# Kernel tuning notes

Measured on AMD Instinct MI355X. Metric: run time of the kernel, lower is better.

## Reference

```python
import jax, jax.numpy as jnp
import numpy as np

B, S, H, E = 4, 4096, 4096, 64
EPS = 1e-6


def setup_inputs() -> dict:
    key = jax.random.key(0)
    k1, k2 = jax.random.split(key)
    hidden_states = jax.random.normal(k1, (B, S, H), dtype=jnp.float32)
    gate_w = jax.random.normal(k2, (E, H), dtype=jnp.float32) * 0.02
    return {"hidden_states": hidden_states, "gate_w": gate_w, "C": 512}


def reference(hidden_states, gate_w, C):
    b, s, h = hidden_states.shape
    e = gate_w.shape[0]
    flat = hidden_states.reshape(-1, h)                    # [BS, H]
    logits = jnp.einsum('th,eh->te', flat, gate_w)          # [BS, E]
    # deterministic=True -> no noise added
    probs = jax.nn.softmax(logits, axis=-1)                 # [BS, E]
    # expert-choice: each expert picks top-C tokens
    _, topC_idx = jax.lax.top_k(logits.T, C)                # [E, C] token indices
    routing_map = jnp.zeros_like(logits).at[
        topC_idx, jnp.arange(e)[:, None]].set(1.0)          # [BS, E]
    # normalize_weights=True
    probs = probs * routing_map
    probs = probs / (probs.sum(axis=-1, keepdims=True) + EPS)
    # aux losses (torch .std() is unbiased -> ddof=1)
    importance = probs.sum(axis=0)                          # [E]
    imp_loss = (jnp.std(importance, ddof=1) / (importance.mean() + EPS)) ** 2
    load = routing_map.sum(axis=0)                          # [E]
    load_loss = (jnp.std(load, ddof=1) / (load.mean() + EPS)) ** 2
    aux_loss = imp_loss + load_loss
    return (probs.reshape(b, s, e), routing_map.reshape(b, s, e), aux_loss)
```

## Files before the change

kernel.cpp:

```cpp
#include <hip/hip_runtime.h>
#include <hip/hip_bf16.h>

#define BS 16384
#define HDIM 4096
#define NE 64
#define KC 64
#define TT 32
#define CAP 512
#define DELTA 2e-3f

typedef __bf16 bf16x8 __attribute__((ext_vector_type(8)));
typedef float f32x4 __attribute__((ext_vector_type(4)));
union Frag { uint4 q; bf16x8 v; };

__device__ inline unsigned f2key(float f) {
    unsigned u = __float_as_uint(f);
    return (u & 0x80000000u) ? ~u : (u | 0x80000000u);
}
__device__ inline float key2f(unsigned k) {
    unsigned u = (k & 0x80000000u) ? (k ^ 0x80000000u) : ~k;
    return __uint_as_float(u);
}
__device__ inline unsigned pack_hi(float a, float b) {
    return (__float_as_uint(a) >> 16) | (__float_as_uint(b) & 0xFFFF0000u);
}
__device__ inline float bf16_resid(float a) {
    return a - __uint_as_float(__float_as_uint(a) & 0xFFFF0000u);
}

__global__ __launch_bounds__(256) void k0_init(const float* __restrict__ W,
                                               unsigned short* __restrict__ Wh,
                                               unsigned short* __restrict__ Wl,
                                               unsigned long long* __restrict__ win_t) {
    const int gtid = blockIdx.x * 256 + threadIdx.x;
    const size_t f = (size_t)gtid * 4;
    float4 w = *(const float4*)(W + f);
    uint2 hh, ll;
    hh.x = pack_hi(w.x, w.y); hh.y = pack_hi(w.z, w.w);
    ll.x = pack_hi(bf16_resid(w.x), bf16_resid(w.y));
    ll.y = pack_hi(bf16_resid(w.z), bf16_resid(w.w));
    *(uint2*)(Wh + f) = hh;
    *(uint2*)(Wl + f) = ll;
    if (gtid < BS) win_t[gtid] = 0ull;
}

__global__ __launch_bounds__(256, 2) void k1_gemm(const float* __restrict__ A,
                                                  const unsigned short* __restrict__ Wh,
                                                  const unsigned short* __restrict__ Wl,
                                                  float* __restrict__ Lg,
                                                  unsigned* __restrict__ KeyT) {
    __shared__ __align__(16) unsigned short sbuf[2 * 13824];

    const int tid = threadIdx.x;
    const int T0 = blockIdx.x * TT;

    const int arow = tid >> 3, aseg = tid & 7;

    const int lane = tid & 63, w = tid >> 6;
    const int m = lane & 15, q = lane >> 4;
    const int wm = w & 1;
    const int wn = w >> 1;

    const float* Aprow = A + (size_t)(T0 + arow) * HDIM + aseg * 8;

    f32x4 acc[2] = {{0.f, 0.f, 0.f, 0.f}, {0.f, 0.f, 0.f, 0.f}};

    float4 pa0 = *(const float4*)(Aprow);
    float4 pa1 = *(const float4*)(Aprow + 4);
    uint4 pwh[2], pwl[2];
#pragma unroll
    for (int i = 0; i < 2; ++i) {
        const int u = i * 256 + tid;
        const int r = u >> 3, blk = u & 7;
        pwh[i] = *(const uint4*)(Wh + (size_t)r * HDIM + blk * 8);
        pwl[i] = *(const uint4*)(Wl + (size_t)r * HDIM + blk * 8);
    }

    {
        unsigned short* B = sbuf;
        uint4 H, L;
        H.x = pack_hi(pa0.x, pa0.y); H.y = pack_hi(pa0.z, pa0.w);
        H.z = pack_hi(pa1.x, pa1.y); H.w = pack_hi(pa1.z, pa1.w);
        L.x = pack_hi(bf16_resid(pa0.x), bf16_resid(pa0.y));
        L.y = pack_hi(bf16_resid(pa0.z), bf16_resid(pa0.w));
        L.z = pack_hi(bf16_resid(pa1.x), bf16_resid(pa1.y));
        L.w = pack_hi(bf16_resid(pa1.z), bf16_resid(pa1.w));
        *(uint4*)(B + arow * 72 + aseg * 8) = H;
        *(uint4*)(B + 2304 + arow * 72 + aseg * 8) = L;
#pragma unroll
        for (int i = 0; i < 2; ++i) {
            const int u = i * 256 + tid;
            const int r = u >> 3, blk = u & 7;
            *(uint4*)(B + 4608 + r * 72 + blk * 8) = pwh[i];
            *(uint4*)(B + 9216 + r * 72 + blk * 8) = pwl[i];
        }
    }

    for (int c = 0; c < HDIM / KC; ++c) {
        if (c + 1 < HDIM / KC) {
            const int c0 = (c + 1) * KC;
            pa0 = *(const float4*)(Aprow + c0);
            pa1 = *(const float4*)(Aprow + c0 + 4);
#pragma unroll
            for (int i = 0; i < 2; ++i) {
                const int u = i * 256 + tid;
                const int r = u >> 3, blk = u & 7;
                pwh[i] = *(const uint4*)(Wh + (size_t)r * HDIM + c0 + blk * 8);
                pwl[i] = *(const uint4*)(Wl + (size_t)r * HDIM + c0 + blk * 8);
            }
        }
        __syncthreads();
        {
            const unsigned short* B = sbuf + (c & 1) * 13824;
            const unsigned short* Ash = B + (wm * 16 + m) * 72;
            const unsigned short* Asl = Ash + 2304;
#pragma unroll
            for (int kh = 0; kh < 2; ++kh) {
                const int ko = kh * 32 + q * 8;
                Frag ah, al;
                ah.q = *(const uint4*)(Ash + ko);
                al.q = *(const uint4*)(Asl + ko);
#pragma unroll
                for (int nt = 0; nt < 2; ++nt) {
                    const int er = wn * 32 + nt * 16 + m;
                    Frag bh, bl;
                    bh.q = *(const uint4*)(B + 4608 + er * 72 + ko);
                    bl.q = *(const uint4*)(B + 9216 + er * 72 + ko);
                    acc[nt] = __builtin_amdgcn_mfma_f32_16x16x32_bf16(ah.v, bh.v, acc[nt], 0, 0, 0);
                    acc[nt] = __builtin_amdgcn_mfma_f32_16x16x32_bf16(al.v, bh.v, acc[nt], 0, 0, 0);
                    acc[nt] = __builtin_amdgcn_mfma_f32_16x16x32_bf16(ah.v, bl.v, acc[nt], 0, 0, 0);
                }
            }
        }
        if (c + 1 < HDIM / KC) {
            unsigned short* B = sbuf + ((c + 1) & 1) * 13824;
            uint4 H, L;
            H.x = pack_hi(pa0.x, pa0.y); H.y = pack_hi(pa0.z, pa0.w);
            H.z = pack_hi(pa1.x, pa1.y); H.w = pack_hi(pa1.z, pa1.w);
            L.x = pack_hi(bf16_resid(pa0.x), bf16_resid(pa0.y));
            L.y = pack_hi(bf16_resid(pa0.z), bf16_resid(pa0.w));
            L.z = pack_hi(bf16_resid(pa1.x), bf16_resid(pa1.y));
            L.w = pack_hi(bf16_resid(pa1.z), bf16_resid(pa1.w));
            *(uint4*)(B + arow * 72 + aseg * 8) = H;
            *(uint4*)(B + 2304 + arow * 72 + aseg * 8) = L;
#pragma unroll
            for (int i = 0; i < 2; ++i) {
                const int u = i * 256 + tid;
                const int r = u >> 3, blk = u & 7;
                *(uint4*)(B + 4608 + r * 72 + blk * 8) = pwh[i];
                *(uint4*)(B + 9216 + r * 72 + blk * 8) = pwl[i];
            }
        }
    }

    __syncthreads();
    float* Sc = (float*)sbuf;
#pragma unroll
    for (int nt = 0; nt < 2; ++nt) {
        const int e = wn * 32 + nt * 16 + m;
#pragma unroll
        for (int r = 0; r < 4; ++r) {
            const int tl = wm * 16 + q * 4 + r;
            const float v = acc[nt][r];
            Sc[tl * 68 + e] = v;
            Lg[(size_t)(T0 + tl) * NE + e] = v;
        }
    }
    __syncthreads();
    {
        const int e = tid >> 2, jj = tid & 3;
        unsigned kk[8];
#pragma unroll
        for (int r = 0; r < 8; ++r) kk[r] = f2key(Sc[(jj * 8 + r) * 68 + e]);
        uint4 v0 = {kk[0], kk[1], kk[2], kk[3]}, v1 = {kk[4], kk[5], kk[6], kk[7]};
        unsigned* dst = KeyT + (size_t)e * BS + T0 + jj * 8;
        *(uint4*)dst = v0;
        *(uint4*)(dst + 4) = v1;
    }
}

__global__ __launch_bounds__(1024) void k2_select(const unsigned* __restrict__ KeyT,
                                                  const int* __restrict__ Cptr,
                                                  unsigned* __restrict__ khi_g,
                                                  int* __restrict__ needed_g,
                                                  int* __restrict__ ncand_g,
                                                  int* __restrict__ cand_g) {
    const int e = blockIdx.x, tid = threadIdx.x;
    const int wid = tid >> 6, lane = tid & 63;
    const int C = *Cptr;
    const unsigned* col = KeyT + (size_t)e * BS;

    unsigned key[16];
#pragma unroll
    for (int j = 0; j < 16; ++j) key[j] = col[j * 1024 + tid];

    __shared__ int sred[16];
    __shared__ int s_tot;
    __shared__ int s_nc;

    unsigned K = 0;
    for (int b = 31; b >= 0; --b) {
        const unsigned T = K | (1u << b);
        int c = 0;
#pragma unroll
        for (int j = 0; j < 16; ++j) c += (key[j] >= T);
#pragma unroll
        for (int off = 32; off; off >>= 1) c += __shfl_xor(c, off);
        if (lane == 0) sred[wid] = c;
        __syncthreads();
        if (wid == 0) {
            int v = (lane < 16) ? sred[lane] : 0;
            v += __shfl_xor(v, 1); v += __shfl_xor(v, 2);
            v += __shfl_xor(v, 4); v += __shfl_xor(v, 8);
            if (lane == 0) s_tot = v;
        }
        __syncthreads();
        if (s_tot >= C) K = T;
        __syncthreads();
    }

    const float vT = key2f(K);
    const unsigned khi = f2key(vT + DELTA);
    const unsigned klo = f2key(vT - DELTA);

    int nd = 0;
#pragma unroll
    for (int j = 0; j < 16; ++j) nd += (key[j] > khi);
#pragma unroll
    for (int off = 32; off; off >>= 1) nd += __shfl_xor(nd, off);
    if (lane == 0) sred[wid] = nd;
    if (tid == 0) s_nc = 0;
    __syncthreads();
    if (wid == 0) {
        int v = (lane < 16) ? sred[lane] : 0;
        v += __shfl_xor(v, 1); v += __shfl_xor(v, 2);
        v += __shfl_xor(v, 4); v += __shfl_xor(v, 8);
        if (lane == 0) s_tot = v;
    }
    __syncthreads();
#pragma unroll
    for (int j = 0; j < 16; ++j) {
        if (key[j] >= klo && key[j] <= khi) {
            const int pos = atomicAdd(&s_nc, 1);
            if (pos < CAP) cand_g[(size_t)e * CAP + pos] = j * 1024 + tid;
        }
    }
    __syncthreads();
    if (tid == 0) {
        khi_g[e] = khi;
        needed_g[e] = C - s_tot;
        ncand_g[e] = (s_nc < CAP) ? s_nc : CAP;
    }
}

__global__ __launch_bounds__(256) void k2b_resolve(const float* __restrict__ A,
                                                   const float* __restrict__ W,
                                                   const int* __restrict__ needed_g,
                                                   const int* __restrict__ ncand_g,
                                                   const int* __restrict__ cand_g,
                                                   unsigned long long* __restrict__ win_t) {
    const int e = blockIdx.x, tid = threadIdx.x, w = tid >> 6, lane = tid & 63;
    int n = ncand_g[e]; if (n > CAP) n = CAP;
    int need = needed_g[e]; if (need > n) need = n; if (need < 0) need = 0;
    __shared__ double sval[CAP];
    __shared__ int sidx[CAP];
    const float* Wr = W + (size_t)e * HDIM;
    for (int c = w; c < n; c += 4) {
        const int t = cand_g[(size_t)e * CAP + c];
        const float* Ar = A + (size_t)t * HDIM;
        double ps = 0.0;
#pragma unroll 8
        for (int j = 0; j < HDIM / 64; ++j)
            ps += (double)Ar[j * 64 + lane] * (double)Wr[j * 64 + lane];
#pragma unroll
        for (int off = 32; off; off >>= 1) ps += __shfl_xor(ps, off);
        if (lane == 0) { sval[c] = ps; sidx[c] = t; }
    }
    __syncthreads();
    if (tid == 0) {
        for (int s = 0; s < need; ++s) {
            int best = -1;
            for (int c = 0; c < n; ++c) {
                if (sidx[c] < 0) continue;
                if (best < 0 || sval[c] > sval[best] ||
                    (sval[c] == sval[best] && sidx[c] < sidx[best]))
                    best = c;
            }
            const int t = sidx[best];
            atomicOr(&win_t[t], 1ull << e);
            sidx[best] = -1;
        }
    }
}

__global__ __launch_bounds__(256) void k3_softmax(const float* __restrict__ Lg,
                                                  const unsigned* __restrict__ khi_g,
                                                  const unsigned long long* __restrict__ win_t,
                                                  float* __restrict__ probs,
                                                  float* __restrict__ out_map,
                                                  double* __restrict__ imp_partial) {
    const int tid = threadIdx.x, w = tid >> 6, e = tid & 63, b = blockIdx.x;
    __shared__ unsigned skhi[64];
    __shared__ double sim[4][64];
    if (tid < 64) skhi[tid] = khi_g[tid];
    __syncthreads();
    const unsigned kh = skhi[e];
    double accim = 0.0;
#pragma unroll
    for (int it = 0; it < 16; ++it) {
        const int t = b * 64 + it * 4 + w;
        const float x = Lg[(size_t)t * NE + e];
        const unsigned key = f2key(x);
        float mfl;
        if (key > kh) mfl = 1.f;
        else mfl = (float)((win_t[t] >> e) & 1ull);
        const float ev = expf(x);
        const float evm = ev * mfl;
        float s1 = ev, s2 = evm;
#pragma unroll
        for (int off = 32; off; off >>= 1) {
            s1 += __shfl_xor(s1, off);
            s2 += __shfl_xor(s2, off);
        }
        const float o = evm / (s2 + 1e-6f * s1);
        probs[(size_t)t * NE + e] = o;
        out_map[(size_t)t * NE + e] = mfl;
        accim += (double)o;
    }
    sim[w][e] = accim;
    __syncthreads();
    if (w == 0)
        imp_partial[(size_t)b * NE + e] = sim[0][e] + sim[1][e] + sim[2][e] + sim[3][e];
}

__global__ __launch_bounds__(64) void k4_aux(const double* __restrict__ imp_partial,
                                             float* __restrict__ out_aux) {
    const int e = threadIdx.x;
    double v = 0.0;
    for (int b = 0; b < 256; ++b) v += imp_partial[(size_t)b * NE + e];
    double s = v;
#pragma unroll
    for (int off = 32; off; off >>= 1) s += __shfl_xor(s, off);
    const double mean = s / 64.0;
    const double d = v - mean;
    double ss = d * d;
#pragma unroll
    for (int off = 32; off; off >>= 1) ss += __shfl_xor(ss, off);
    if (e == 0) {
        const double var = ss / 63.0;
        const double dn = mean + 1e-6;
        out_aux[0] = (float)(var / (dn * dn));
    }
}

extern "C" void kernel_launch(void* const* d_in, const int* in_sizes, int n_in,
                              void* d_out, int out_size, void* d_ws, size_t ws_size,
                              hipStream_t stream) {
    const float* A = (const float*)d_in[0];
    const float* W = (const float*)d_in[1];
    const int* Cptr = (const int*)d_in[2];

    float* out_probs = (float*)d_out;
    float* out_map = out_probs + (size_t)BS * NE;
    float* out_aux = out_map + (size_t)BS * NE;

    char* wsb = (char*)d_ws;
    float*              Lg     = (float*)wsb;
    unsigned*           KeyT   = (unsigned*)(wsb + (4ull << 20));
    unsigned short*     Wh     = (unsigned short*)(wsb + (8ull << 20));
    unsigned short*     Wl     = (unsigned short*)(wsb + (8ull << 20) + (512ull << 10));
    int*                cand   = (int*)(wsb + (9ull << 20));
    unsigned long long* win_t  = (unsigned long long*)(wsb + (9ull << 20) + (128ull << 10));
    unsigned*           khi_g  = (unsigned*)(wsb + (9ull << 20) + (256ull << 10));
    int*                needed = (int*)(wsb + (9ull << 20) + (257ull << 10));
    int*                ncand  = (int*)(wsb + (9ull << 20) + (258ull << 10));
    double*             imp_p  = (double*)(wsb + (9ull << 20) + (512ull << 10));

    k0_init<<<256, 256, 0, stream>>>(W, Wh, Wl, win_t);
    k1_gemm<<<BS / TT, 256, 0, stream>>>(A, Wh, Wl, Lg, KeyT);
    k2_select<<<NE, 1024, 0, stream>>>(KeyT, Cptr, khi_g, needed, ncand, cand);
    k2b_resolve<<<NE, 256, 0, stream>>>(A, W, needed, ncand, cand, win_t);
    k3_softmax<<<BS / 64, 256, 0, stream>>>(Lg, khi_g, win_t, out_probs, out_map, imp_p);
    k4_aux<<<1, 64, 0, stream>>>(imp_p, out_aux);
}
```

Before: 464.0 us.

## Replace bitwise radix threshold search with single-pass shared-memory histogram

The top-C threshold search in the select kernel no longer runs 32 rounds of count-and-reduce, each with three block barriers. It builds one 16384-bin histogram in shared memory from the high 14 key bits. A suffix scan then finds the bin that holds the C-th largest key, and the candidate window is widened to that bin's value range plus twice the tolerance. This cuts barrier and reduction traffic, but it adds LDS atomics, 64KB of shared memory that limits occupancy, and a wider candidate band that could overflow CAP and push more work into the resolve kernel.

```diff
diff --git a/kernel.cpp b/kernel.cpp
--- a/kernel.cpp
+++ b/kernel.cpp
@@ -190,38 +190,68 @@
     const int C = *Cptr;
     const unsigned* col = KeyT + (size_t)e * BS;
 
+    __shared__ unsigned hist[16384];
+    __shared__ int wtot[16], wab[16];
+    __shared__ int sred[16];
+    __shared__ int s_B, s_nc, s_tot;
+
     unsigned key[16];
 #pragma unroll
     for (int j = 0; j < 16; ++j) key[j] = col[j * 1024 + tid];
 
-    __shared__ int sred[16];
-    __shared__ int s_tot;
-    __shared__ int s_nc;
-
-    unsigned K = 0;
-    for (int b = 31; b >= 0; --b) {
-        const unsigned T = K | (1u << b);
-        int c = 0;
-#pragma unroll
-        for (int j = 0; j < 16; ++j) c += (key[j] >= T);
-#pragma unroll
-        for (int off = 32; off; off >>= 1) c += __shfl_xor(c, off);
-        if (lane == 0) sred[wid] = c;
-        __syncthreads();
-        if (wid == 0) {
-            int v = (lane < 16) ? sred[lane] : 0;
-            v += __shfl_xor(v, 1); v += __shfl_xor(v, 2);
-            v += __shfl_xor(v, 4); v += __shfl_xor(v, 8);
-            if (lane == 0) s_tot = v;
-        }
-        __syncthreads();
-        if (s_tot >= C) K = T;
-        __syncthreads();
-    }
-
-    const float vT = key2f(K);
-    const unsigned khi = f2key(vT + DELTA);
-    const unsigned klo = f2key(vT - DELTA);
+    {
+        uint4 z = {0, 0, 0, 0};
+#pragma unroll
+        for (int i = 0; i < 4; ++i) *(uint4*)&hist[(i * 1024 + tid) * 4] = z;
+    }
+    if (tid == 0) { s_nc = 0; s_B = 0; }
+    __syncthreads();
+
+#pragma unroll
+    for (int j = 0; j < 16; ++j) atomicAdd(&hist[key[j] >> 18], 1u);
+    __syncthreads();
+
+    int loc = 0;
+#pragma unroll
+    for (int k = 0; k < 16; ++k) loc += (int)hist[tid * 16 + k];
+
+    int sfx = loc;
+#pragma unroll
+    for (int off = 1; off < 64; off <<= 1) {
+        const int v = __shfl_down(sfx, off);
+        if (lane + off < 64) sfx += v;
+    }
+    if (lane == 0) wtot[wid] = sfx;
+    __syncthreads();
+    if (wid == 0 && lane < 16) {
+        int v = wtot[lane];
+        int s = v;
+#pragma unroll
+        for (int off = 1; off < 16; off <<= 1) {
+            const int u = __shfl_down(s, off);
+            if (lane + off < 16) s += u;
+        }
+        wab[lane] = s - v;
+    }
+    __syncthreads();
+
+    const int cum_incl = sfx + wab[wid];
+    const int cum_excl = cum_incl - loc;
+    if (cum_excl < C && cum_incl >= C) {
+        int run = cum_excl;
+        for (int k = 15; k >= 0; --k) {
+            run += (int)hist[tid * 16 + k];
+            if (run >= C) { s_B = tid * 16 + k; break; }
+        }
+    }
+    __syncthreads();
+
+    const int B = s_B;
+    const float vlo = key2f((unsigned)B << 18);
+    unsigned khi;
+    if (B >= 16383) khi = 0xFFFFFFFFu;
+    else khi = f2key(key2f((unsigned)(B + 1) << 18) + 2.0f * DELTA);
+    const unsigned klo = f2key(vlo - 2.0f * DELTA);
 
     int nd = 0;
 #pragma unroll
@@ -229,7 +259,6 @@
 #pragma unroll
     for (int off = 32; off; off >>= 1) nd += __shfl_xor(nd, off);
     if (lane == 0) sred[wid] = nd;
-    if (tid == 0) s_nc = 0;
     __syncthreads();
     if (wid == 0) {
         int v = (lane < 16) ? sred[lane] : 0;
@@ -237,7 +266,6 @@
         v += __shfl_xor(v, 4); v += __shfl_xor(v, 8);
         if (lane == 0) s_tot = v;
     }
-    __syncthreads();
 #pragma unroll
     for (int j = 0; j < 16; ++j) {
         if (key[j] >= klo && key[j] <= khi) {
```

After: 907.2 us. +95.5%, slower.
